# Optimization experiments

Measured on AMD Instinct MI355X. Metric: run time of the kernel, lower is better.

## Reference

```python
import jax, jax.numpy as jnp
import numpy as np
from jax import lax

K = 50            # n_segments in original SLIC call
ITERS = 10        # SLIC k-means iterations (skimage default max_num_iter=10)
COMPACTNESS = 10.0  # skimage SLIC default compactness


def _slic_weights(img):
    """SLIC-style superpixel segmentation of img [H,W,3] -> per-pixel weight 1/|segment|.

    Faithful to the module's use of skimage.slic: k-means in joint (color, xy)
    space with spatial coords scaled by compactness/S, S = sqrt(H*W/K),
    grid-initialized centers, then weight[p] = 1/count(segment[p]).
    """
    H, W, _ = img.shape
    N = H * W
    S = float(np.sqrt(N / K))
    ratio = COMPACTNESS / S
    yy, xx = jnp.meshgrid(jnp.arange(H, dtype=img.dtype),
                          jnp.arange(W, dtype=img.dtype), indexing='ij')
    feats = jnp.concatenate(
        [img.reshape(N, 3), (jnp.stack([yy, xx], -1).reshape(N, 2)) * ratio],
        axis=-1)  # [N,5]

    # grid-initialized centers (static shapes -> numpy at trace time)
    n = int(np.ceil(np.sqrt(K)))
    cy = ((np.arange(n) + 0.5) * H / n).astype(np.int64)
    cx = ((np.arange(n) + 0.5) * W / n).astype(np.int64)
    gy, gx = np.meshgrid(cy, cx, indexing='ij')
    init_idx = jnp.asarray((gy * W + gx).reshape(-1)[:K])
    centers0 = feats[init_idx]  # [K,5]

    f2 = jnp.sum(feats * feats, axis=-1)  # [N]

    def assign(centers):
        # squared distances via expansion: avoids [N,K,5] intermediate
        c2 = jnp.sum(centers * centers, axis=-1)            # [K]
        d = f2[:, None] + c2[None, :] - 2.0 * feats @ centers.T  # [N,K]
        return jnp.argmin(d, axis=1)

    def step(centers, _):
        lab = assign(centers)
        sums = jax.ops.segment_sum(feats, lab, num_segments=K)
        cnts = jax.ops.segment_sum(jnp.ones((N,), feats.dtype), lab, num_segments=K)
        new_centers = sums / jnp.maximum(cnts, 1.0)[:, None]
        return new_centers, None

    centers, _ = lax.scan(step, centers0, None, length=ITERS)
    lab = assign(centers)                                   # [N]
    cnts = jax.ops.segment_sum(jnp.ones((N,), feats.dtype), lab, num_segments=K)
    w = (1.0 / jnp.maximum(cnts, 1.0))[lab]                 # [N], 1/|segment|
    return w.reshape(H, W)


def setup_inputs() -> dict:
    key = jax.random.key(0)
    x = jax.random.uniform(key, (16, 3, 512, 512), dtype=jnp.float32)
    return {"x": x}


def reference(x):
    # per-pixel segment weights (computed from detached data in the original)
    w = lax.stop_gradient(jax.vmap(_slic_weights)(x.transpose(0, 2, 3, 1)))  # [B,H,W]
    xw = x * w[:, None, :, :]                    # broadcast over RGB channels
    mean_rgb = jnp.mean(xw, axis=(2, 3), keepdims=True)  # [B,3,1,1]
    mr = mean_rgb[:, 0:1]
    mg = mean_rgb[:, 1:2]
    mb = mean_rgb[:, 2:3]
    Drg = (mr - mg) ** 2
    Drb = (mr - mb) ** 2
    Dgb = (mb - mg) ** 2
    k = jnp.sqrt(Drg ** 2 + Drb ** 2 + Dgb ** 2)  # [B,1,1,1]
    return k
```

## Files before the change

kernel.cpp:

```cpp
#include <hip/hip_runtime.h>
#include <cmath>

#define K_SEG 50
#define ITERS 10
#define NPASS (ITERS + 1)
#define H_IMG 512
#define W_IMG 512
#define NPIX (H_IMG * W_IMG)
#define BATCH 16
#define SLOTS (K_SEG * 6)
#define TOTAL_SLOTS (NPASS * BATCH * SLOTS)


__global__ void zero_all(double* __restrict__ g) {
    int i = blockIdx.x * 256 + threadIdx.x;
    if (i < TOTAL_SLOTS) g[i] = 0.0;
}

__global__ void __launch_bounds__(256) assign_fused(
        const float* __restrict__ x, double* __restrict__ gsums,
        int it, float ratiof) {
    __shared__ float cen[K_SEG][6];
    __shared__ float cmax[K_SEG];
    __shared__ double part[K_SEG][6];
    __shared__ int klist4[4][52];
    __shared__ int ncand4[4];

    int t = threadIdx.x;
    int tx = blockIdx.x, ty = blockIdx.y, b = blockIdx.z;
    const float* xb = x + (size_t)b * 3 * NPIX;

    if (it == 0) {
        if (t < K_SEG) {
            int i = t >> 3, j = t & 7;
            int y = 32 + 64 * i, xc = 32 + 64 * j;
            int p = y * W_IMG + xc;
            float r = xb[p], g = xb[NPIX + p], bl = xb[2 * NPIX + p];
            float cfy = (float)y * ratiof, cfx = (float)xc * ratiof;
            cen[t][0]=r; cen[t][1]=g; cen[t][2]=bl; cen[t][3]=cfy; cen[t][4]=cfx;
            cen[t][5] = 0.5f * ((((r*r + g*g) + bl*bl) + cfy*cfy) + cfx*cfx);
            float m0 = fmaxf(r, 1.0f - r), m1 = fmaxf(g, 1.0f - g), m2 = fmaxf(bl, 1.0f - bl);
            cmax[t] = (m0*m0 + m1*m1) + m2*m2;
        }
    } else {
        const double* gp = gsums + ((size_t)(it - 1) * BATCH + b) * SLOTS;
        for (int i = t; i < SLOTS; i += 256) ((double*)part)[i] = gp[i];
        __syncthreads();
        if (t < K_SEG) {
            double cv = part[t][5];
            double denom = cv > 1.0 ? cv : 1.0;
            double rcp = 1.0 / denom;
            float c0 = (float)(part[t][0] * rcp);
            float c1 = (float)(part[t][1] * rcp);
            float c2v = (float)(part[t][2] * rcp);
            float c3 = (float)(part[t][3] * rcp);
            float c4 = (float)(part[t][4] * rcp);
            cen[t][0]=c0; cen[t][1]=c1; cen[t][2]=c2v; cen[t][3]=c3; cen[t][4]=c4;
            cen[t][5] = 0.5f * ((((c0*c0 + c1*c1) + c2v*c2v) + c3*c3) + c4*c4);
            float m0 = fmaxf(c0, 1.0f - c0), m1 = fmaxf(c1, 1.0f - c1), m2 = fmaxf(c2v, 1.0f - c2v);
            cmax[t] = (m0*m0 + m1*m1) + m2*m2;
        }
    }
    __syncthreads();

    int wid = t >> 6;
    int lane = t & 63;
    {
        float Rmin = INFINITY, val = INFINITY;
        if (lane < K_SEG) {
            float cy = cen[lane][3], cxx = cen[lane][4];
            float y0 = (float)(ty * 64 + wid * 16) * ratiof;
            float y1 = (float)(ty * 64 + wid * 16 + 15) * ratiof;
            float x0 = (float)(tx * 64) * ratiof;
            float x1 = (float)(tx * 64 + 63) * ratiof;
            float dyn = fmaxf(fmaxf(y0 - cy, cy - y1), 0.0f);
            float dxn = fmaxf(fmaxf(x0 - cxx, cxx - x1), 0.0f);
            float dyf = fmaxf(cy - y0, y1 - cy);
            float dxf = fmaxf(cxx - x0, x1 - cxx);
            Rmin = dyn * dyn + dxn * dxn;
            val = (dyf * dyf + dxf * dxf) + cmax[lane];
        }
        float u = val;
        for (int off = 32; off; off >>= 1) u = fminf(u, __shfl_xor(u, off));
        bool cand = (lane < K_SEG) && (Rmin <= u + 0.25f);
        unsigned long long m = __ballot(cand);
        if (cand) {
            int pos = __popcll(m & ((1ull << lane) - 1ull));
            klist4[wid][pos] = lane;
        }
        if (lane == 0) ncand4[wid] = __popcll(m);
    }
    for (int i = t; i < SLOTS; i += 256) ((double*)part)[i] = 0.0;
    __syncthreads();
    int nc = ncand4[wid];

    int row = t >> 2;
    int colq = (t & 3) << 4;
    int gy = ty * 64 + row;
    int gx0 = tx * 64 + colq;
    float fy = (float)gy * ratiof;

    int runlab = -1;
    float sr = 0.0f, sg = 0.0f, sb = 0.0f, scol = 0.0f;
    int rn = 0;
    for (int h = 0; h < 2; ++h) {
        int gx = gx0 + h * 8;
        size_t p = (size_t)gy * W_IMG + gx;
        float4 ra = *(const float4*)(xb + p);
        float4 rb4 = *(const float4*)(xb + p + 4);
        float4 ga = *(const float4*)(xb + NPIX + p);
        float4 gb4 = *(const float4*)(xb + NPIX + p + 4);
        float4 ba = *(const float4*)(xb + 2 * NPIX + p);
        float4 bb4 = *(const float4*)(xb + 2 * NPIX + p + 4);
        float rr[8] = {ra.x, ra.y, ra.z, ra.w, rb4.x, rb4.y, rb4.z, rb4.w};
        float gg[8] = {ga.x, ga.y, ga.z, ga.w, gb4.x, gb4.y, gb4.z, gb4.w};
        float bv[8] = {ba.x, ba.y, ba.z, ba.w, bb4.x, bb4.y, bb4.z, bb4.w};
        float fx8[8], best8[8];
        int lab8[8];
#pragma unroll
        for (int u2 = 0; u2 < 8; ++u2) {
            fx8[u2] = (float)(gx + u2) * ratiof;
            best8[u2] = INFINITY;
            lab8[u2] = 0;
        }
        for (int c = 0; c < nc; ++c) {
            int k = klist4[wid][c];
            float c0 = cen[k][0], c1 = cen[k][1], c2v = cen[k][2];
            float c3 = cen[k][3], c4 = cen[k][4], h2 = cen[k][5];
            float base = fmaf(fy, -c3, h2);
#pragma unroll
            for (int u2 = 0; u2 < 8; ++u2) {
                float s = fmaf(rr[u2], -c0, base);
                s = fmaf(gg[u2], -c1, s);
                s = fmaf(bv[u2], -c2v, s);
                s = fmaf(fx8[u2], -c4, s);
                if (s < best8[u2]) { best8[u2] = s; lab8[u2] = k; }
            }
        }
#pragma unroll
        for (int u2 = 0; u2 < 8; ++u2) {
            if (lab8[u2] != runlab) {
                if (rn > 0) {
                    double* pp = part[runlab];
                    unsafeAtomicAdd(&pp[0], (double)sr);
                    unsafeAtomicAdd(&pp[1], (double)sg);
                    unsafeAtomicAdd(&pp[2], (double)sb);
                    unsafeAtomicAdd(&pp[3], (double)((float)(gy * rn)));
                    unsafeAtomicAdd(&pp[4], (double)scol);
                    unsafeAtomicAdd(&pp[5], (double)rn);
                }
                runlab = lab8[u2];
                sr = rr[u2]; sg = gg[u2]; sb = bv[u2]; scol = (float)(gx + u2); rn = 1;
            } else {
                sr += rr[u2]; sg += gg[u2]; sb += bv[u2]; scol += (float)(gx + u2); rn += 1;
            }
        }
    }

    {
        float fsr = sr, fsg = sg, fsb = sb, fscol = scol;
        float fsrow = (float)(gy * rn);
        float frn = (float)rn;
        unsigned long long remaining = __ballot(true);
        while (remaining) {
            int leader = __ffsll((unsigned long long)remaining) - 1;
            int labL = __shfl(runlab, leader);
            bool in = (runlab == labL);
            unsigned long long grp = __ballot(in);
            float a0 = in ? fsr : 0.0f, a1 = in ? fsg : 0.0f, a2 = in ? fsb : 0.0f;
            float a3 = in ? fsrow : 0.0f, a4 = in ? fscol : 0.0f, a5 = in ? frn : 0.0f;
#pragma unroll
            for (int off = 1; off < 64; off <<= 1) {
                a0 += __shfl_xor(a0, off);
                a1 += __shfl_xor(a1, off);
                a2 += __shfl_xor(a2, off);
                a3 += __shfl_xor(a3, off);
                a4 += __shfl_xor(a4, off);
                a5 += __shfl_xor(a5, off);
            }
            if (lane == leader) {
                double* pp = part[labL];
                unsafeAtomicAdd(&pp[0], (double)a0);
                unsafeAtomicAdd(&pp[1], (double)a1);
                unsafeAtomicAdd(&pp[2], (double)a2);
                unsafeAtomicAdd(&pp[3], (double)a3);
                unsafeAtomicAdd(&pp[4], (double)a4);
                unsafeAtomicAdd(&pp[5], (double)a5);
            }
            remaining &= ~grp;
        }
    }
    __syncthreads();

    double* gp = gsums + ((size_t)it * BATCH + b) * SLOTS;
    for (int i = t; i < SLOTS; i += 256) {
        double v = ((double*)part)[i];
        int slot = i % 6;
        if (slot == 3 || slot == 4) v *= (double)ratiof;
        if (v != 0.0) unsafeAtomicAdd(&gp[i], v);
    }
}

__global__ void finalize_kernel(const double* __restrict__ gsums, float* __restrict__ out) {
    int t = threadIdx.x;
    if (t < BATCH) {
        const double* gp = gsums + ((size_t)ITERS * BATCH + t) * SLOTS;
        double sr = 0.0, sg = 0.0, sb = 0.0;
        for (int k = 0; k < K_SEG; ++k) {
            const double* s = gp + k * 6;
            double cv = s[5];
            float cntf = (float)(cv > 1.0 ? cv : 1.0);
            float wf = 1.0f / cntf;
            sr += s[0] * (double)wf;
            sg += s[1] * (double)wf;
            sb += s[2] * (double)wf;
        }
        double mr = sr / (double)NPIX, mg = sg / (double)NPIX, mb = sb / (double)NPIX;
        double Drg = (mr - mg) * (mr - mg);
        double Drb = (mr - mb) * (mr - mb);
        double Dgb = (mb - mg) * (mb - mg);
        out[t] = (float)sqrt(Drg * Drg + Drb * Drb + Dgb * Dgb);
    }
}


__global__ void init_kernelF(const float* __restrict__ x, double* __restrict__ gsums,
                             float* __restrict__ centers, float* __restrict__ c2s,
                             float ratiof) {
    int b = blockIdx.x;
    int t = threadIdx.x;
    for (int i = t; i < SLOTS; i += blockDim.x) gsums[b * SLOTS + i] = 0.0;
    if (t < K_SEG) {
        int i = t >> 3, j = t & 7;
        int y = 32 + 64 * i, xc = 32 + 64 * j;
        const float* xb = x + (size_t)b * 3 * NPIX;
        int p = y * W_IMG + xc;
        float r = xb[p], g = xb[NPIX + p], bl = xb[2 * NPIX + p];
        float fyc = (float)y * ratiof, fxc = (float)xc * ratiof;
        float* c = centers + (b * K_SEG + t) * 5;
        c[0] = r; c[1] = g; c[2] = bl; c[3] = fyc; c[4] = fxc;
        c2s[b * K_SEG + t] = (((r * r + g * g) + bl * bl) + fyc * fyc) + fxc * fxc;
    }
}

__global__ void __launch_bounds__(128, 4) assign_kernelF(
        const float* __restrict__ x, double* __restrict__ gsums,
        const float* __restrict__ centers, const float* __restrict__ c2s,
        float ratiof) {
    __shared__ float cen[K_SEG][5];
    __shared__ float c2l[K_SEG];
    __shared__ double part[K_SEG][6];
    __shared__ int klist[K_SEG];
    __shared__ int ncand_s;

    int t = threadIdx.x;
    int tx = blockIdx.x, ty = blockIdx.y, b = blockIdx.z;

    const float* csrc = centers + b * K_SEG * 5;
    for (int i = t; i < K_SEG * 5; i += 128) ((float*)cen)[i] = csrc[i];
    for (int i = t; i < K_SEG; i += 128) c2l[i] = c2s[b * K_SEG + i];
    for (int i = t; i < SLOTS; i += 128) ((double*)part)[i] = 0.0;
    __syncthreads();

    if (t < 64) {
        int k = t;
        float R = INFINITY, val = INFINITY;
        if (k < K_SEG) {
            float cy = cen[k][3], cx = cen[k][4];
            float y0 = (float)(ty * 32) * ratiof;
            float y1 = (float)(ty * 32 + 31) * ratiof;
            float x0 = (float)(tx * 64) * ratiof;
            float x1 = (float)(tx * 64 + 63) * ratiof;
            float dyn = fmaxf(fmaxf(y0 - cy, cy - y1), 0.0f);
            float dxn = fmaxf(fmaxf(x0 - cx, cx - x1), 0.0f);
            float dyf = fmaxf(cy - y0, y1 - cy);
            float dxf = fmaxf(cx - x0, x1 - cx);
            R = dyn * dyn + dxn * dxn;
            val = (dyf * dyf + dxf * dxf) + 3.0f;
        }
        float u = val;
        for (int off = 32; off; off >>= 1) u = fminf(u, __shfl_xor(u, off));
        bool cand = (k < K_SEG) && (R <= u + 4.0f);
        unsigned long long m = __ballot(cand);
        if (cand) {
            int pos = __popcll(m & ((1ull << t) - 1ull));
            klist[pos] = k;
        }
        if (t == 0) ncand_s = __popcll(m);
    }
    __syncthreads();
    int ncand = ncand_s;

    int row = t >> 2;
    int colq = (t & 3) << 4;
    int gy = ty * 32 + row;
    int gx0 = tx * 64 + colq;
    const float* xb = x + (size_t)b * 3 * NPIX;
    float fy = (float)gy * ratiof;

    int runlab = -1;
    float sr = 0.0f, sg = 0.0f, sb = 0.0f, sfx = 0.0f;
    int rn = 0;

    for (int h = 0; h < 2; ++h) {
        int gx = gx0 + h * 8;
        size_t p = (size_t)gy * W_IMG + gx;
        float4 ra = *(const float4*)(xb + p);
        float4 rb4 = *(const float4*)(xb + p + 4);
        float4 ga = *(const float4*)(xb + NPIX + p);
        float4 gb4 = *(const float4*)(xb + NPIX + p + 4);
        float4 ba = *(const float4*)(xb + 2 * NPIX + p);
        float4 bb4 = *(const float4*)(xb + 2 * NPIX + p + 4);
        float rr[8] = {ra.x, ra.y, ra.z, ra.w, rb4.x, rb4.y, rb4.z, rb4.w};
        float gg[8] = {ga.x, ga.y, ga.z, ga.w, gb4.x, gb4.y, gb4.z, gb4.w};
        float bv[8] = {ba.x, ba.y, ba.z, ba.w, bb4.x, bb4.y, bb4.z, bb4.w};
        float fx8[8], f28[8], best8[8];
        int lab8[8];
#pragma unroll
        for (int u2 = 0; u2 < 8; ++u2) {
            fx8[u2] = (float)(gx + u2) * ratiof;
            f28[u2] = (((rr[u2] * rr[u2] + gg[u2] * gg[u2]) + bv[u2] * bv[u2]) + fy * fy) + fx8[u2] * fx8[u2];
            best8[u2] = INFINITY;
            lab8[u2] = 0;
        }
        for (int c = 0; c < ncand; ++c) {
            int k = klist[c];
            float c0 = cen[k][0], c1 = cen[k][1], c2v = cen[k][2], c3 = cen[k][3], c4 = cen[k][4];
            float c2k = c2l[k];
#pragma unroll
            for (int u2 = 0; u2 < 8; ++u2) {
                float dot = rr[u2] * c0 + gg[u2] * c1 + bv[u2] * c2v + fy * c3 + fx8[u2] * c4;
                float d = (f28[u2] + c2k) - 2.0f * dot;
                if (d < best8[u2]) { best8[u2] = d; lab8[u2] = k; }
            }
        }
#pragma unroll
        for (int u2 = 0; u2 < 8; ++u2) {
            if (lab8[u2] != runlab) {
                if (rn > 0) {
                    double* pp = part[runlab];
                    unsafeAtomicAdd(&pp[0], (double)sr);
                    unsafeAtomicAdd(&pp[1], (double)sg);
                    unsafeAtomicAdd(&pp[2], (double)sb);
                    unsafeAtomicAdd(&pp[3], (double)fy * (double)rn);
                    unsafeAtomicAdd(&pp[4], (double)sfx);
                    unsafeAtomicAdd(&pp[5], (double)rn);
                }
                runlab = lab8[u2];
                sr = rr[u2]; sg = gg[u2]; sb = bv[u2]; sfx = fx8[u2]; rn = 1;
            } else {
                sr += rr[u2]; sg += gg[u2]; sb += bv[u2]; sfx += fx8[u2]; rn += 1;
            }
        }
    }
    if (rn > 0) {
        double* pp = part[runlab];
        unsafeAtomicAdd(&pp[0], (double)sr);
        unsafeAtomicAdd(&pp[1], (double)sg);
        unsafeAtomicAdd(&pp[2], (double)sb);
        unsafeAtomicAdd(&pp[3], (double)fy * (double)rn);
        unsafeAtomicAdd(&pp[4], (double)sfx);
        unsafeAtomicAdd(&pp[5], (double)rn);
    }
    __syncthreads();
    for (int i = t; i < SLOTS; i += 128) {
        double v = ((double*)part)[i];
        if (v != 0.0) unsafeAtomicAdd(&gsums[b * SLOTS + i], v);
    }
}

__global__ void update_kernelF(double* __restrict__ gsums, float* __restrict__ centers,
                               float* __restrict__ c2s) {
    int b = blockIdx.x;
    int t = threadIdx.x;
    if (t < K_SEG) {
        double* s = gsums + (b * K_SEG + t) * 6;
        double cv = s[5];
        double denom = cv > 1.0 ? cv : 1.0;
        float c[5];
#pragma unroll
        for (int j = 0; j < 5; ++j) { c[j] = (float)(s[j] / denom); s[j] = 0.0; }
        s[5] = 0.0;
        float* cd = centers + (b * K_SEG + t) * 5;
#pragma unroll
        for (int j = 0; j < 5; ++j) cd[j] = c[j];
        c2s[b * K_SEG + t] = (((c[0] * c[0] + c[1] * c[1]) + c[2] * c[2]) + c[3] * c[3]) + c[4] * c[4];
    }
}

__global__ void finalize_kernelF(const double* __restrict__ gsums, float* __restrict__ out) {
    int t = threadIdx.x;
    if (t < BATCH) {
        double sr = 0.0, sg = 0.0, sb = 0.0;
        for (int k = 0; k < K_SEG; ++k) {
            const double* s = gsums + (t * K_SEG + k) * 6;
            double cv = s[5];
            float cntf = (float)(cv > 1.0 ? cv : 1.0);
            float wf = 1.0f / cntf;
            sr += s[0] * (double)wf;
            sg += s[1] * (double)wf;
            sb += s[2] * (double)wf;
        }
        double mr = sr / (double)NPIX, mg = sg / (double)NPIX, mb = sb / (double)NPIX;
        double Drg = (mr - mg) * (mr - mg);
        double Drb = (mr - mb) * (mr - mb);
        double Dgb = (mb - mg) * (mb - mg);
        out[t] = (float)sqrt(Drg * Drg + Drb * Drb + Dgb * Dgb);
    }
}

extern "C" void kernel_launch(void* const* d_in, const int* in_sizes, int n_in,
                              void* d_out, int out_size, void* d_ws, size_t ws_size,
                              hipStream_t stream) {
    const float* x = (const float*)d_in[0];
    float* out = (float*)d_out;
    char* ws = (char*)d_ws;

    double S = sqrt((double)NPIX / (double)K_SEG);
    float ratiof = (float)(10.0 / S);

    if (ws_size >= (size_t)TOTAL_SLOTS * sizeof(double)) {
        double* gsums = (double*)ws;
        zero_all<<<(TOTAL_SLOTS + 255) / 256, 256, 0, stream>>>(gsums);
        dim3 agrid(W_IMG / 64, H_IMG / 64, BATCH);
        for (int it = 0; it < NPASS; ++it)
            assign_fused<<<agrid, 256, 0, stream>>>(x, gsums, it, ratiof);
        finalize_kernel<<<1, 64, 0, stream>>>(gsums, out);
        return;
    }

    const size_t gbytes = (size_t)BATCH * SLOTS * sizeof(double);
    double* gsums = (double*)ws;
    float* centers = (float*)(ws + gbytes);
    float* c2s = (float*)(ws + gbytes + (size_t)BATCH * K_SEG * 5 * 4);

    init_kernelF<<<BATCH, 64, 0, stream>>>(x, gsums, centers, c2s, ratiof);
    dim3 agrid(W_IMG / 64, H_IMG / 32, BATCH);
    for (int it = 0; it < ITERS; ++it) {
        assign_kernelF<<<agrid, 128, 0, stream>>>(x, gsums, centers, c2s, ratiof);
        update_kernelF<<<BATCH, 64, 0, stream>>>(gsums, centers, c2s);
    }
    assign_kernelF<<<agrid, 128, 0, stream>>>(x, gsums, centers, c2s, ratiof);
    finalize_kernelF<<<1, 64, 0, stream>>>(gsums, out);
}
```

Before: 213.7 us.

## Fuse all SLIC passes into one persistent kernel with per-image barriers

Replaces the eleven per-pass launches with a single persistent kernel of 1024 blocks. Each image's 64 blocks synchronise through a global atomic counter and spin-wait between iterations, and finalisation is folded into the kernel. This removes repeated launch overhead and the inter-kernel gaps. In exchange it relies on all blocks being co-resident, checked with an occupancy query, and on a spin barrier that has a timeout escape which could silently break correctness. The old fallback path is also removed.

```diff
diff --git a/kernel.cpp b/kernel.cpp
--- a/kernel.cpp
+++ b/kernel.cpp
@@ -10,26 +10,20 @@
 #define BATCH 16
 #define SLOTS (K_SEG * 6)
 #define TOTAL_SLOTS (NPASS * BATCH * SLOTS)
-
-
-__global__ void zero_all(double* __restrict__ g) {
+#define BLK_PER_IMG 64
+#define GRID_BLKS (BATCH * BLK_PER_IMG)
+
+
+__global__ void zero_ws(unsigned* __restrict__ w, int nwords) {
     int i = blockIdx.x * 256 + threadIdx.x;
-    if (i < TOTAL_SLOTS) g[i] = 0.0;
-}
-
-__global__ void __launch_bounds__(256) assign_fused(
-        const float* __restrict__ x, double* __restrict__ gsums,
-        int it, float ratiof) {
-    __shared__ float cen[K_SEG][6];
-    __shared__ float cmax[K_SEG];
-    __shared__ double part[K_SEG][6];
-    __shared__ int klist4[4][52];
-    __shared__ int ncand4[4];
-
-    int t = threadIdx.x;
-    int tx = blockIdx.x, ty = blockIdx.y, b = blockIdx.z;
-    const float* xb = x + (size_t)b * 3 * NPIX;
-
+    if (i < nwords) w[i] = 0u;
+}
+
+__device__ __forceinline__ void pass_body(
+        const float* __restrict__ xb, double* __restrict__ gsums,
+        int it, int b, int tx, int ty, int t, float ratiof,
+        float (*cen)[6], float* cmax, double (*part)[6],
+        int (*klist4)[52], int* ncand4) {
     if (it == 0) {
         if (t < K_SEG) {
             int i = t >> 3, j = t & 7;
@@ -201,6 +195,74 @@
     }
 }
 
+__global__ void __launch_bounds__(256) persist_light(
+        const float* __restrict__ x, double* __restrict__ gsums,
+        unsigned* __restrict__ cnt, float* __restrict__ out, float ratiof) {
+    __shared__ float cen[K_SEG][6];
+    __shared__ float cmax[K_SEG];
+    __shared__ double part[K_SEG][6];
+    __shared__ int klist4[4][52];
+    __shared__ int ncand4[4];
+
+    int t = threadIdx.x;
+    int blk = blockIdx.x;
+    int b = blk >> 6;
+    int tid6 = blk & 63;
+    int ty = tid6 >> 3, tx = tid6 & 7;
+    const float* xb = x + (size_t)b * 3 * NPIX;
+
+    for (int it = 0; it < NPASS; ++it) {
+        pass_body(xb, gsums, it, b, tx, ty, t, ratiof, cen, cmax, part, klist4, ncand4);
+
+        if (t == 0) {
+            unsigned* c = &cnt[it * BATCH + b];
+            __threadfence();
+            __hip_atomic_fetch_add(c, 1u, __ATOMIC_ACQ_REL, __HIP_MEMORY_SCOPE_AGENT);
+            unsigned spins = 0;
+            while (__hip_atomic_load(c, __ATOMIC_ACQUIRE, __HIP_MEMORY_SCOPE_AGENT)
+                   < (unsigned)BLK_PER_IMG) {
+                __builtin_amdgcn_s_sleep(2);
+                if (++spins > (1u << 22)) break;
+            }
+        }
+        __syncthreads();
+    }
+
+    if (tid6 == 0 && t == 0) {
+        const double* gp = gsums + ((size_t)ITERS * BATCH + b) * SLOTS;
+        double sr = 0.0, sg = 0.0, sb = 0.0;
+        for (int k = 0; k < K_SEG; ++k) {
+            const double* s = gp + k * 6;
+            double cv = s[5];
+            float cntf = (float)(cv > 1.0 ? cv : 1.0);
+            float wf = 1.0f / cntf;
+            sr += s[0] * (double)wf;
+            sg += s[1] * (double)wf;
+            sb += s[2] * (double)wf;
+        }
+        double mr = sr / (double)NPIX, mg = sg / (double)NPIX, mb = sb / (double)NPIX;
+        double Drg = (mr - mg) * (mr - mg);
+        double Drb = (mr - mb) * (mr - mb);
+        double Dgb = (mb - mg) * (mb - mg);
+        out[b] = (float)sqrt(Drg * Drg + Drb * Drb + Dgb * Dgb);
+    }
+}
+
+
+__global__ void __launch_bounds__(256) assign_fused(
+        const float* __restrict__ x, double* __restrict__ gsums,
+        int it, float ratiof) {
+    __shared__ float cen[K_SEG][6];
+    __shared__ float cmax[K_SEG];
+    __shared__ double part[K_SEG][6];
+    __shared__ int klist4[4][52];
+    __shared__ int ncand4[4];
+    int t = threadIdx.x;
+    int tx = blockIdx.x, ty = blockIdx.y, b = blockIdx.z;
+    const float* xb = x + (size_t)b * 3 * NPIX;
+    pass_body(xb, gsums, it, b, tx, ty, t, ratiof, cen, cmax, part, klist4, ncand4);
+}
+
 __global__ void finalize_kernel(const double* __restrict__ gsums, float* __restrict__ out) {
     int t = threadIdx.x;
     if (t < BATCH) {
@@ -223,192 +285,6 @@
     }
 }
 
-
-__global__ void init_kernelF(const float* __restrict__ x, double* __restrict__ gsums,
-                             float* __restrict__ centers, float* __restrict__ c2s,
-                             float ratiof) {
-    int b = blockIdx.x;
-    int t = threadIdx.x;
-    for (int i = t; i < SLOTS; i += blockDim.x) gsums[b * SLOTS + i] = 0.0;
-    if (t < K_SEG) {
-        int i = t >> 3, j = t & 7;
-        int y = 32 + 64 * i, xc = 32 + 64 * j;
-        const float* xb = x + (size_t)b * 3 * NPIX;
-        int p = y * W_IMG + xc;
-        float r = xb[p], g = xb[NPIX + p], bl = xb[2 * NPIX + p];
-        float fyc = (float)y * ratiof, fxc = (float)xc * ratiof;
-        float* c = centers + (b * K_SEG + t) * 5;
-        c[0] = r; c[1] = g; c[2] = bl; c[3] = fyc; c[4] = fxc;
-        c2s[b * K_SEG + t] = (((r * r + g * g) + bl * bl) + fyc * fyc) + fxc * fxc;
-    }
-}
-
-__global__ void __launch_bounds__(128, 4) assign_kernelF(
-        const float* __restrict__ x, double* __restrict__ gsums,
-        const float* __restrict__ centers, const float* __restrict__ c2s,
-        float ratiof) {
-    __shared__ float cen[K_SEG][5];
-    __shared__ float c2l[K_SEG];
-    __shared__ double part[K_SEG][6];
-    __shared__ int klist[K_SEG];
-    __shared__ int ncand_s;
-
-    int t = threadIdx.x;
-    int tx = blockIdx.x, ty = blockIdx.y, b = blockIdx.z;
-
-    const float* csrc = centers + b * K_SEG * 5;
-    for (int i = t; i < K_SEG * 5; i += 128) ((float*)cen)[i] = csrc[i];
-    for (int i = t; i < K_SEG; i += 128) c2l[i] = c2s[b * K_SEG + i];
-    for (int i = t; i < SLOTS; i += 128) ((double*)part)[i] = 0.0;
-    __syncthreads();
-
-    if (t < 64) {
-        int k = t;
-        float R = INFINITY, val = INFINITY;
-        if (k < K_SEG) {
-            float cy = cen[k][3], cx = cen[k][4];
-            float y0 = (float)(ty * 32) * ratiof;
-            float y1 = (float)(ty * 32 + 31) * ratiof;
-            float x0 = (float)(tx * 64) * ratiof;
-            float x1 = (float)(tx * 64 + 63) * ratiof;
-            float dyn = fmaxf(fmaxf(y0 - cy, cy - y1), 0.0f);
-            float dxn = fmaxf(fmaxf(x0 - cx, cx - x1), 0.0f);
-            float dyf = fmaxf(cy - y0, y1 - cy);
-            float dxf = fmaxf(cx - x0, x1 - cx);
-            R = dyn * dyn + dxn * dxn;
-            val = (dyf * dyf + dxf * dxf) + 3.0f;
-        }
-        float u = val;
-        for (int off = 32; off; off >>= 1) u = fminf(u, __shfl_xor(u, off));
-        bool cand = (k < K_SEG) && (R <= u + 4.0f);
-        unsigned long long m = __ballot(cand);
-        if (cand) {
-            int pos = __popcll(m & ((1ull << t) - 1ull));
-            klist[pos] = k;
-        }
-        if (t == 0) ncand_s = __popcll(m);
-    }
-    __syncthreads();
-    int ncand = ncand_s;
-
-    int row = t >> 2;
-    int colq = (t & 3) << 4;
-    int gy = ty * 32 + row;
-    int gx0 = tx * 64 + colq;
-    const float* xb = x + (size_t)b * 3 * NPIX;
-    float fy = (float)gy * ratiof;
-
-    int runlab = -1;
-    float sr = 0.0f, sg = 0.0f, sb = 0.0f, sfx = 0.0f;
-    int rn = 0;
-
-    for (int h = 0; h < 2; ++h) {
-        int gx = gx0 + h * 8;
-        size_t p = (size_t)gy * W_IMG + gx;
-        float4 ra = *(const float4*)(xb + p);
-        float4 rb4 = *(const float4*)(xb + p + 4);
-        float4 ga = *(const float4*)(xb + NPIX + p);
-        float4 gb4 = *(const float4*)(xb + NPIX + p + 4);
-        float4 ba = *(const float4*)(xb + 2 * NPIX + p);
-        float4 bb4 = *(const float4*)(xb + 2 * NPIX + p + 4);
-        float rr[8] = {ra.x, ra.y, ra.z, ra.w, rb4.x, rb4.y, rb4.z, rb4.w};
-        float gg[8] = {ga.x, ga.y, ga.z, ga.w, gb4.x, gb4.y, gb4.z, gb4.w};
-        float bv[8] = {ba.x, ba.y, ba.z, ba.w, bb4.x, bb4.y, bb4.z, bb4.w};
-        float fx8[8], f28[8], best8[8];
-        int lab8[8];
-#pragma unroll
-        for (int u2 = 0; u2 < 8; ++u2) {
-            fx8[u2] = (float)(gx + u2) * ratiof;
-            f28[u2] = (((rr[u2] * rr[u2] + gg[u2] * gg[u2]) + bv[u2] * bv[u2]) + fy * fy) + fx8[u2] * fx8[u2];
-            best8[u2] = INFINITY;
-            lab8[u2] = 0;
-        }
-        for (int c = 0; c < ncand; ++c) {
-            int k = klist[c];
-            float c0 = cen[k][0], c1 = cen[k][1], c2v = cen[k][2], c3 = cen[k][3], c4 = cen[k][4];
-            float c2k = c2l[k];
-#pragma unroll
-            for (int u2 = 0; u2 < 8; ++u2) {
-                float dot = rr[u2] * c0 + gg[u2] * c1 + bv[u2] * c2v + fy * c3 + fx8[u2] * c4;
-                float d = (f28[u2] + c2k) - 2.0f * dot;
-                if (d < best8[u2]) { best8[u2] = d; lab8[u2] = k; }
-            }
-        }
-#pragma unroll
-        for (int u2 = 0; u2 < 8; ++u2) {
-            if (lab8[u2] != runlab) {
-                if (rn > 0) {
-                    double* pp = part[runlab];
-                    unsafeAtomicAdd(&pp[0], (double)sr);
-                    unsafeAtomicAdd(&pp[1], (double)sg);
-                    unsafeAtomicAdd(&pp[2], (double)sb);
-                    unsafeAtomicAdd(&pp[3], (double)fy * (double)rn);
-                    unsafeAtomicAdd(&pp[4], (double)sfx);
-                    unsafeAtomicAdd(&pp[5], (double)rn);
-                }
-                runlab = lab8[u2];
-                sr = rr[u2]; sg = gg[u2]; sb = bv[u2]; sfx = fx8[u2]; rn = 1;
-            } else {
-                sr += rr[u2]; sg += gg[u2]; sb += bv[u2]; sfx += fx8[u2]; rn += 1;
-            }
-        }
-    }
-    if (rn > 0) {
-        double* pp = part[runlab];
-        unsafeAtomicAdd(&pp[0], (double)sr);
-        unsafeAtomicAdd(&pp[1], (double)sg);
-        unsafeAtomicAdd(&pp[2], (double)sb);
-        unsafeAtomicAdd(&pp[3], (double)fy * (double)rn);
-        unsafeAtomicAdd(&pp[4], (double)sfx);
-        unsafeAtomicAdd(&pp[5], (double)rn);
-    }
-    __syncthreads();
-    for (int i = t; i < SLOTS; i += 128) {
-        double v = ((double*)part)[i];
-        if (v != 0.0) unsafeAtomicAdd(&gsums[b * SLOTS + i], v);
-    }
-}
-
-__global__ void update_kernelF(double* __restrict__ gsums, float* __restrict__ centers,
-                               float* __restrict__ c2s) {
-    int b = blockIdx.x;
-    int t = threadIdx.x;
-    if (t < K_SEG) {
-        double* s = gsums + (b * K_SEG + t) * 6;
-        double cv = s[5];
-        double denom = cv > 1.0 ? cv : 1.0;
-        float c[5];
-#pragma unroll
-        for (int j = 0; j < 5; ++j) { c[j] = (float)(s[j] / denom); s[j] = 0.0; }
-        s[5] = 0.0;
-        float* cd = centers + (b * K_SEG + t) * 5;
-#pragma unroll
-        for (int j = 0; j < 5; ++j) cd[j] = c[j];
-        c2s[b * K_SEG + t] = (((c[0] * c[0] + c[1] * c[1]) + c[2] * c[2]) + c[3] * c[3]) + c[4] * c[4];
-    }
-}
-
-__global__ void finalize_kernelF(const double* __restrict__ gsums, float* __restrict__ out) {
-    int t = threadIdx.x;
-    if (t < BATCH) {
-        double sr = 0.0, sg = 0.0, sb = 0.0;
-        for (int k = 0; k < K_SEG; ++k) {
-            const double* s = gsums + (t * K_SEG + k) * 6;
-            double cv = s[5];
-            float cntf = (float)(cv > 1.0 ? cv : 1.0);
-            float wf = 1.0f / cntf;
-            sr += s[0] * (double)wf;
-            sg += s[1] * (double)wf;
-            sb += s[2] * (double)wf;
-        }
-        double mr = sr / (double)NPIX, mg = sg / (double)NPIX, mb = sb / (double)NPIX;
-        double Drg = (mr - mg) * (mr - mg);
-        double Drb = (mr - mb) * (mr - mb);
-        double Dgb = (mb - mg) * (mb - mg);
-        out[t] = (float)sqrt(Drg * Drg + Drb * Drb + Dgb * Dgb);
-    }
-}
-
 extern "C" void kernel_launch(void* const* d_in, const int* in_sizes, int n_in,
                               void* d_out, int out_size, void* d_ws, size_t ws_size,
                               hipStream_t stream) {
@@ -419,27 +295,30 @@
     double S = sqrt((double)NPIX / (double)K_SEG);
     float ratiof = (float)(10.0 / S);
 
-    if (ws_size >= (size_t)TOTAL_SLOTS * sizeof(double)) {
+    const size_t gbytes = (size_t)TOTAL_SLOTS * sizeof(double);
+    const size_t need = gbytes + (size_t)NPASS * BATCH * sizeof(unsigned);
+
+    int dev = 0, ncu = 0, occ = 0;
+    (void)hipGetDevice(&dev);
+    (void)hipDeviceGetAttribute(&ncu, hipDeviceAttributeMultiprocessorCount, dev);
+    (void)hipOccupancyMaxActiveBlocksPerMultiprocessor(&occ, persist_light, 256, 0);
+
+    if ((long)occ * (long)ncu >= GRID_BLKS && ws_size >= need) {
         double* gsums = (double*)ws;
-        zero_all<<<(TOTAL_SLOTS + 255) / 256, 256, 0, stream>>>(gsums);
+        unsigned* cnt = (unsigned*)(ws + gbytes);
+        int nwords = (int)(need / 4);
+        zero_ws<<<(nwords + 255) / 256, 256, 0, stream>>>((unsigned*)ws, nwords);
+        persist_light<<<GRID_BLKS, 256, 0, stream>>>(x, gsums, cnt, out, ratiof);
+        return;
+    }
+
+    if (ws_size >= gbytes) {
+        double* gsums = (double*)ws;
+        int nwords = (int)(gbytes / 4);
+        zero_ws<<<(nwords + 255) / 256, 256, 0, stream>>>((unsigned*)ws, nwords);
         dim3 agrid(W_IMG / 64, H_IMG / 64, BATCH);
         for (int it = 0; it < NPASS; ++it)
             assign_fused<<<agrid, 256, 0, stream>>>(x, gsums, it, ratiof);
         finalize_kernel<<<1, 64, 0, stream>>>(gsums, out);
-        return;
-    }
-
-    const size_t gbytes = (size_t)BATCH * SLOTS * sizeof(double);
-    double* gsums = (double*)ws;
-    float* centers = (float*)(ws + gbytes);
-    float* c2s = (float*)(ws + gbytes + (size_t)BATCH * K_SEG * 5 * 4);
-
-    init_kernelF<<<BATCH, 64, 0, stream>>>(x, gsums, centers, c2s, ratiof);
-    dim3 agrid(W_IMG / 64, H_IMG / 32, BATCH);
-    for (int it = 0; it < ITERS; ++it) {
-        assign_kernelF<<<agrid, 128, 0, stream>>>(x, gsums, centers, c2s, ratiof);
-        update_kernelF<<<BATCH, 64, 0, stream>>>(gsums, centers, c2s);
-    }
-    assign_kernelF<<<agrid, 128, 0, stream>>>(x, gsums, centers, c2s, ratiof);
-    finalize_kernelF<<<1, 64, 0, stream>>>(gsums, out);
-}
+    }
+}
```

Result: no change. 213.1 us (-0.3%).
